# Kernel optimization log

Hardware: AMD Instinct MI355X
Metric: run time of the kernel (lower is better)

Reference implementation:

```python
import jax, jax.numpy as jnp
import numpy as np

GROUPS = 32
EPS = 1e-6

def group_norm(x, gamma, beta):
    # x: [B,C,H,W]
    B, C, H, W = x.shape
    xg = x.reshape(B, GROUPS, C // GROUPS, H, W)
    mu = xg.mean(axis=(2, 3, 4), keepdims=True)
    var = xg.var(axis=(2, 3, 4), keepdims=True)
    xn = ((xg - mu) * jax.lax.rsqrt(var + EPS)).reshape(B, C, H, W)
    return xn * gamma[None, :, None, None] + beta[None, :, None, None]

def setup_inputs() -> dict:
    key = jax.random.key(0)
    ks = jax.random.split(key, 12)
    B, C, H, W = 4, 256, 64, 64
    s = 1.0 / np.sqrt(C)
    return {
        "x": jax.random.normal(ks[0], (B, C, H, W), jnp.float32),
        "gn_gamma": jnp.ones((C,), jnp.float32),
        "gn_beta": jnp.zeros((C,), jnp.float32),
        "wq": jax.random.normal(ks[1], (C, C), jnp.float32) * s,
        "bq": jnp.zeros((C,), jnp.float32),
        "wk": jax.random.normal(ks[2], (C, C), jnp.float32) * s,
        "bk": jnp.zeros((C,), jnp.float32),
        "wv": jax.random.normal(ks[3], (C, C), jnp.float32) * s,
        "bv": jnp.zeros((C,), jnp.float32),
        "wu": jax.random.normal(ks[4], (1, C), jnp.float32) * s,
        "bu": jnp.zeros((1,), jnp.float32),
        "wp": jax.random.normal(ks[5], (C, C), jnp.float32) * s,
        "bp": jnp.zeros((C,), jnp.float32),
    }

def reference(x, gn_gamma, gn_beta, wq, bq, wk, bk, wv, bv, wu, bu, wp, bp):
    B, C, H, W = x.shape
    hw = H * W
    hn = group_norm(x, gn_gamma, gn_beta)          # norm(x); context=x so same norm
    t = hn.reshape(B, C, hw).transpose(0, 2, 1)    # [B, hw, C]
    q = t @ wq.T + bq                              # 1x1 conv == per-token linear
    k = t @ wk.T + bk
    v = t @ wv.T + bv
    u_map = jax.nn.sigmoid(t @ wu.T + bu)          # [B, hw, 1]
    scale = jnp.asarray(C, x.dtype) ** -0.5
    scores = jnp.einsum('bic,bjc->bij', q, k) * scale * u_map.transpose(0, 2, 1)
    attn = jax.nn.softmax(scores, axis=2)          # softmax over keys j
    out = jnp.einsum('bij,bjc->bic', attn, v)      # [B, hw, C]
    out = (out @ wp.T + bp).transpose(0, 2, 1).reshape(B, C, H, W)
    return (x + out, u_map)
```

## Files before the change

### kernel.cpp

```cpp
#include <hip/hip_runtime.h>
#include <cstdint>

#define B_ 4
#define C_ 256
#define HW_ 4096
#define CPG_ 8
#define M_TOT 16384
#define SCALE 0.0625f
#define LOG2E 1.44269504088896f
#define FLASH_LDS 133120

typedef __attribute__((ext_vector_type(4))) float f32x4;
typedef __attribute__((ext_vector_type(16))) float f32x16;
typedef __attribute__((ext_vector_type(8))) unsigned short u16x8;
typedef __attribute__((ext_vector_type(4))) unsigned short u16x4;
typedef __attribute__((ext_vector_type(4))) unsigned int u32x4;
typedef __attribute__((ext_vector_type(8))) __bf16 bf16x8;

static __device__ __forceinline__ unsigned short f2bf(float f) {
  unsigned int u = __builtin_bit_cast(unsigned int, f);
  u += 0x7fffu + ((u >> 16) & 1u);
  return (unsigned short)(u >> 16);
}
static __device__ __forceinline__ float bf2f(unsigned short s) {
  return __builtin_bit_cast(float, ((unsigned int)s) << 16);
}
static __device__ __forceinline__ bf16x8 ldbf8(const unsigned short* p) {
  return __builtin_bit_cast(bf16x8, *(const u16x8*)p);
}
static __device__ __forceinline__ bf16x8 cvt8(const float* p) {
  f32x4 a = *(const f32x4*)p;
  f32x4 b = *(const f32x4*)(p + 4);
  u16x8 r;
  r[0] = f2bf(a[0]); r[1] = f2bf(a[1]); r[2] = f2bf(a[2]); r[3] = f2bf(a[3]);
  r[4] = f2bf(b[0]); r[5] = f2bf(b[1]); r[6] = f2bf(b[2]); r[7] = f2bf(b[3]);
  return __builtin_bit_cast(bf16x8, r);
}
static __device__ __forceinline__ void gload16(const void* g, void* l) {
  __builtin_amdgcn_global_load_lds(
      (const __attribute__((address_space(1))) unsigned int*)g,
      (__attribute__((address_space(3))) unsigned int*)l, 16, 0, 0);
}
static __device__ __forceinline__ unsigned cvtpk(float lo, float hi) {
  unsigned r;
  asm("v_cvt_pk_bf16_f32 %0, %1, %2" : "=v"(r) : "v"(lo), "v"(hi));
  return r;
}

__global__ __launch_bounds__(256) void gn_kernel(const float* __restrict__ x,
    const float* __restrict__ gamma, const float* __restrict__ beta,
    unsigned short* __restrict__ t) {
  int bg = blockIdx.x;
  int b = bg >> 5, g = bg & 31;
  const float* xp = x + ((size_t)(b * C_ + g * CPG_)) * HW_;
  float s = 0.f, ss = 0.f;
  for (int i = threadIdx.x; i < CPG_ * HW_; i += 256) {
    float v = xp[i]; s += v; ss += v * v;
  }
#pragma unroll
  for (int m = 32; m; m >>= 1) { s += __shfl_xor(s, m); ss += __shfl_xor(ss, m); }
  __shared__ float red[8];
  if ((threadIdx.x & 63) == 0) { red[threadIdx.x >> 6] = s; red[4 + (threadIdx.x >> 6)] = ss; }
  __syncthreads();
  float S = red[0] + red[1] + red[2] + red[3];
  float SS = red[4] + red[5] + red[6] + red[7];
  float mean = S * (1.f / 32768.f);
  float var = SS * (1.f / 32768.f) - mean * mean;
  float rs = rsqrtf(var + 1e-6f);
  float gam[CPG_], bet[CPG_];
#pragma unroll
  for (int cc = 0; cc < CPG_; ++cc) {
    float gm = gamma[g * CPG_ + cc];
    gam[cc] = gm * rs;
    bet[cc] = beta[g * CPG_ + cc] - mean * gm * rs;
  }
  for (int sp = threadIdx.x; sp < HW_; sp += 256) {
    u16x8 o;
#pragma unroll
    for (int cc = 0; cc < CPG_; ++cc) {
      float v = xp[cc * HW_ + sp];
      o[cc] = f2bf(v * gam[cc] + bet[cc]);
    }
    *(u16x8*)(t + ((size_t)(b * HW_ + sp)) * C_ + g * CPG_) = o;
  }
}

__global__ __launch_bounds__(256) void u_kernel(const unsigned short* __restrict__ t,
    const float* __restrict__ wu, const float* __restrict__ bu,
    float* __restrict__ uout) {
  int w = threadIdx.x >> 6, l = threadIdx.x & 63;
  int tok = blockIdx.x * 4 + w;
  u16x4 tv = *(const u16x4*)(t + (size_t)tok * C_ + l * 4);
  f32x4 wv4 = *(const f32x4*)(wu + l * 4);
  float d = bf2f(tv[0]) * wv4[0] + bf2f(tv[1]) * wv4[1] +
            bf2f(tv[2]) * wv4[2] + bf2f(tv[3]) * wv4[3];
#pragma unroll
  for (int m = 32; m; m >>= 1) d += __shfl_xor(d, m);
  if (l == 0) uout[tok] = 1.f / (1.f + __expf(-(d + bu[0])));
}

__global__ __launch_bounds__(256, 2) void qkv_kernel(const unsigned short* __restrict__ t,
    const float* __restrict__ wq, const float* __restrict__ wk, const float* __restrict__ wv,
    const float* __restrict__ bq, const float* __restrict__ bk, const float* __restrict__ bv,
    const float* __restrict__ uu,
    unsigned short* __restrict__ q, unsigned short* __restrict__ k,
    unsigned short* __restrict__ vt) {
  int mblk = blockIdx.x, nblk = blockIdx.y;
  int n0 = nblk * 64;
  __shared__ unsigned short WL[64][264];
  __shared__ float lds[64][65];
  int tid = threadIdx.x;
  int wid = tid >> 6, l = tid & 63;
  int lr = l & 15, lg = l >> 4;
  int row = mblk * 64 + wid * 16 + lr;
  bf16x8 af[8];
  const unsigned short* ap = t + (size_t)row * C_ + lg * 8;
#pragma unroll
  for (int kc = 0; kc < 8; ++kc) af[kc] = ldbf8(ap + kc * 32);
  f32x4 u4 = *(const f32x4*)(uu + mblk * 64 + wid * 16 + lg * 4);

#pragma unroll 1
  for (int w = 0; w < 3; ++w) {
    const float* W = w == 0 ? wq : (w == 1 ? wk : wv);
    const float* bias = w == 0 ? bq : (w == 1 ? bk : bv);
    if (w) __syncthreads();
#pragma unroll
    for (int p = 0; p < 8; ++p) {
      int rw = p * 8 + (tid >> 5);
      int kc0 = (tid & 31) * 8;
      *(bf16x8*)&WL[rw][kc0] = cvt8(W + (size_t)(n0 + rw) * C_ + kc0);
    }
    __syncthreads();
    f32x4 acc[4] = {};
#pragma unroll
    for (int kc = 0; kc < 8; ++kc)
#pragma unroll
      for (int j = 0; j < 4; ++j) {
        bf16x8 bb = ldbf8(&WL[j * 16 + lr][kc * 32 + lg * 8]);
        acc[j] = __builtin_amdgcn_mfma_f32_16x16x32_bf16(af[kc], bb, acc[j], 0, 0, 0);
      }
    if (w < 2) {
      unsigned short* dst = w ? k : q;
      float su[4] = {1.f, 1.f, 1.f, 1.f};
      if (w == 1) {
        su[0] = SCALE * LOG2E * u4[0]; su[1] = SCALE * LOG2E * u4[1];
        su[2] = SCALE * LOG2E * u4[2]; su[3] = SCALE * LOG2E * u4[3];
      }
#pragma unroll
      for (int j = 0; j < 4; ++j) {
        int col = n0 + j * 16 + lr;
        float bv_ = bias[col];
#pragma unroll
        for (int r = 0; r < 4; ++r)
          dst[(size_t)(mblk * 64 + wid * 16 + lg * 4 + r) * C_ + col] =
              f2bf((acc[j][r] + bv_) * su[r]);
      }
    } else {
#pragma unroll
      for (int j = 0; j < 4; ++j) {
        float bv_ = bias[n0 + j * 16 + lr];
#pragma unroll
        for (int r = 0; r < 4; ++r)
          lds[wid * 16 + lg * 4 + r][j * 16 + lr] = acc[j][r] + bv_;
      }
      __syncthreads();
      int bb_ = (mblk * 64) >> 12;
      int s0 = (mblk * 64) & 4095;
      int ss = tid & 63, cc0 = tid >> 6;
      for (int cc = cc0; cc < 64; cc += 4)
        vt[((size_t)(bb_ * C_ + n0 + cc)) * HW_ + s0 + ss] = f2bf(lds[ss][cc]);
    }
  }
}

__global__ __launch_bounds__(512, 2) void flash_kernel(const unsigned short* __restrict__ q,
    const unsigned short* __restrict__ k, const unsigned short* __restrict__ vt,
    unsigned short* __restrict__ o) {
  extern __shared__ char smem[];
  float* cmb_m = (float*)(smem + 131072);
  float* cmb_l = (float*)(smem + 131584);
  float* facw  = (float*)(smem + 132096);
  float* scrL  = (float*)(smem + 132608);

  int blk = blockIdx.x;
  int xcd = blk & 7, slot = blk >> 3;
  int b = xcd >> 1;
  int qrow0 = (((xcd & 1) << 5) | slot) * 64;
  int tid = threadIdx.x;
  int wid = tid >> 6, l = tid & 63;
  int l5 = l & 31, hi = l >> 5;

  const unsigned short* kb = k + (size_t)b * HW_ * C_;
  const unsigned short* vb = vt + (size_t)b * C_ * HW_;

  float mrow = -1e30f, lrow = 0.f;
  f32x16 oa[8];

  if (wid >= 4) {
    int role = wid - 4;
    int sh = role & 1;
    bool isK = role < 2;
    int w_ = l >> 2;
    int w0_ = w_ & 1, w1_ = (w_ >> 1) & 1, w2_ = (w_ >> 2) & 1, w3_ = (w_ >> 3) & 1;
    int koffb = (l & 3) * 8;
#define STG(IT, BUFN)                                                           \
    {                                                                           \
      int key0n = sh * 2048 + (IT) * 32;                                        \
      if (isK) {                                                                \
        _Pragma("unroll")                                                       \
        for (int j = 0; j < 16; ++j) {                                          \
          int key = j * 2 + hi;                                                 \
          const unsigned short* g =                                             \
              kb + (size_t)(key0n + key) * C_ + ((l5 * 8) ^ (key * 8));         \
          gload16(g, smem + (BUFN) * 32768 + sh * 16384 + j * 1024);            \
        }                                                                       \
      } else {                                                                  \
        _Pragma("unroll")                                                       \
        for (int j = 0; j < 16; ++j) {                                          \
          int j0 = j & 1;                                                       \
          int ch = (j << 4) | (w3_ << 3) | ((w2_ ^ j0) << 2) |                  \
                   ((w1_ ^ w3_) << 1) | (w0_ ^ w2_ ^ j0);                       \
          int ke = koffb ^ ((ch & 3) << 3);                                     \
          const unsigned short* g = vb + (size_t)ch * HW_ + key0n + ke;         \
          gload16(g, smem + 65536 + (BUFN) * 32768 + sh * 16384 + j * 1024);    \
        }                                                                       \
      }                                                                         \
    }
    STG(0, 0);
    __syncthreads();
    for (int it = 0; it < 64; ++it) {
      if (it + 1 < 64) STG(it + 1, (it + 1) & 1);
      __syncthreads();
    }
#undef STG
  } else {
    int h = wid >> 1, qs = wid & 1;
    bf16x8 qreg[16];
    {
      const unsigned short* qp =
          q + ((size_t)b * HW_ + qrow0 + qs * 32 + l5) * C_ + hi * 8;
#pragma unroll
      for (int cc = 0; cc < 16; ++cc) qreg[cc] = ldbf8(qp + cc * 16);
    }
#pragma unroll
    for (int ct = 0; ct < 8; ++ct)
#pragma unroll
      for (int r = 0; r < 16; ++r) oa[ct][r] = 0.f;
    __syncthreads();

    int kx = l5 << 4;
    int vbase = (l5 * 64) ^ ((l5 >> 2) << 6);
    int ko0 = (hi * 16) ^ ((l & 3) << 4);
    int ko1 = (32 + hi * 16) ^ ((l & 3) << 4);

    for (int it = 0; it < 64; ++it) {
      int buf = it & 1;
      const char* KB = smem + buf * 32768 + h * 16384;
      f32x16 sa, sb;
#pragma unroll
      for (int r = 0; r < 16; ++r) { sa[r] = 0.f; sb[r] = 0.f; }
#pragma unroll
      for (int cc = 0; cc < 16; cc += 2) {
        bf16x8 kf0 = ldbf8((const unsigned short*)(KB + l5 * 512 +
                                                   ((cc * 32 + hi * 16) ^ kx)));
        bf16x8 kf1 = ldbf8((const unsigned short*)(KB + l5 * 512 +
                                                   (((cc + 1) * 32 + hi * 16) ^ kx)));
        sa = __builtin_amdgcn_mfma_f32_32x32x16_bf16(kf0, qreg[cc], sa, 0, 0, 0);
        sb = __builtin_amdgcn_mfma_f32_32x32x16_bf16(kf1, qreg[cc + 1], sb, 0, 0, 0);
      }
      f32x16 s = sa + sb;
      float mxl = s[0];
#pragma unroll
      for (int r = 1; r < 16; ++r) mxl = fmaxf(mxl, s[r]);
      float mx = fmaxf(mxl, __shfl_xor(mxl, 32));
      if (!__all(mx <= mrow + 11.f)) {
        float mnew = fmaxf(mrow, mx);
        float scr = exp2f(mrow - mnew);
        mrow = mnew;
        lrow *= scr;
        if (hi == 0) scrL[wid * 32 + l5] = scr;
        float sr[16];
#pragma unroll
        for (int r = 0; r < 16; ++r)
          sr[r] = scrL[wid * 32 + (r & 3) + 8 * (r >> 2) + 4 * hi];
#pragma unroll
        for (int ct = 0; ct < 8; ++ct)
#pragma unroll
          for (int r = 0; r < 16; ++r) oa[ct][r] *= sr[r];
      }
      unsigned wp[8];
#pragma unroll
      for (int rp = 0; rp < 8; ++rp) {
        float e0 = exp2f(s[2 * rp] - mrow);
        float e1 = exp2f(s[2 * rp + 1] - mrow);
        lrow += e0 + e1;
        wp[rp] = cvtpk(e0, e1);
      }
      unsigned sx[8];
#pragma unroll
      for (int rp = 0; rp < 8; ++rp) sx[rp] = (unsigned)__shfl_xor((int)wp[rp], 32);
      bool hib = (hi != 0);
      u32x4 pa0u = {hib ? sx[2] : wp[0], hib ? sx[3] : wp[1],
                    hib ? wp[2] : sx[0], hib ? wp[3] : sx[1]};
      u32x4 pa1u = {hib ? sx[6] : wp[4], hib ? sx[7] : wp[5],
                    hib ? wp[6] : sx[4], hib ? wp[7] : sx[5]};
      bf16x8 pa0 = __builtin_bit_cast(bf16x8, pa0u);
      bf16x8 pa1 = __builtin_bit_cast(bf16x8, pa1u);
      const char* VB = smem + 65536 + buf * 32768 + h * 16384;
#pragma unroll
      for (int ct = 0; ct < 8; ++ct) {
        bf16x8 v0 = ldbf8((const unsigned short*)(VB + ct * 2048 + vbase + ko0));
        bf16x8 v1 = ldbf8((const unsigned short*)(VB + ct * 2048 + vbase + ko1));
        oa[ct] = __builtin_amdgcn_mfma_f32_32x32x16_bf16(pa0, v0, oa[ct], 0, 0, 0);
        oa[ct] = __builtin_amdgcn_mfma_f32_32x32x16_bf16(pa1, v1, oa[ct], 0, 0, 0);
      }
      __syncthreads();
    }
  }

  float l_all = 0.f;
  if (wid < 4) {
    l_all = lrow + __shfl_xor(lrow, 32);
    if (hi == 0) { cmb_m[wid * 32 + l5] = mrow; cmb_l[wid * 32 + l5] = l_all; }
  }
  __syncthreads();
  if (wid < 4) {
    float mo = cmb_m[(wid ^ 2) * 32 + l5];
    float lo = cmb_l[(wid ^ 2) * 32 + l5];
    float M = fmaxf(mrow, mo);
    float el = exp2f(mrow - M), eo = exp2f(mo - M);
    float fac = el / (l_all * el + lo * eo);
    if (hi == 0) facw[wid * 32 + l5] = fac;
    float fr[16];
#pragma unroll
    for (int r = 0; r < 16; ++r)
      fr[r] = facw[wid * 32 + (r & 3) + 8 * (r >> 2) + 4 * hi];
    float* Ow = (float*)(smem + wid * 32768);
#pragma unroll
    for (int ct = 0; ct < 8; ++ct)
#pragma unroll
      for (int r = 0; r < 16; ++r) {
        int qr = (r & 3) + 8 * (r >> 2) + 4 * hi;
        Ow[qr * 256 + ct * 32 + l5] = oa[ct][r] * fr[r];
      }
  }
  __syncthreads();
  for (int e = tid; e < 2048; e += 512) {
    int row = e >> 5;
    int c8 = (e & 31) * 8;
    int qs_ = row >> 5, q_ = row & 31;
    const float* p0 = (const float*)(smem + qs_ * 32768) + q_ * 256 + c8;
    const float* p1 = (const float*)(smem + (2 + qs_) * 32768) + q_ * 256 + c8;
    u16x8 ov;
#pragma unroll
    for (int j = 0; j < 8; ++j) ov[j] = f2bf(p0[j] + p1[j]);
    *(u16x8*)(o + ((size_t)b * HW_ + qrow0 + row) * C_ + c8) = ov;
  }
}

__global__ __launch_bounds__(256, 2) void proj_kernel(const unsigned short* __restrict__ o,
    const float* __restrict__ wp, const float* __restrict__ bp,
    const float* __restrict__ x, float* __restrict__ y) {
  int mblk = blockIdx.x, nblk = blockIdx.y;
  int n0 = nblk * 64;
  __shared__ unsigned short WL[64][264];
  int tid = threadIdx.x;
#pragma unroll
  for (int p = 0; p < 8; ++p) {
    int row = p * 8 + (tid >> 5);
    int kc0 = (tid & 31) * 8;
    *(bf16x8*)&WL[row][kc0] = cvt8(wp + (size_t)(n0 + row) * C_ + kc0);
  }
  __syncthreads();
  int wid = tid >> 6, l = tid & 63;
  int lr = l & 15, lg = l >> 4;
  int row = mblk * 64 + wid * 16 + lr;
  f32x4 acc[4] = {};
  const unsigned short* ap = o + (size_t)row * C_ + lg * 8;
#pragma unroll
  for (int kc = 0; kc < 8; ++kc) {
    bf16x8 a = ldbf8(ap + kc * 32);
#pragma unroll
    for (int j = 0; j < 4; ++j) {
      bf16x8 bb = ldbf8(&WL[j * 16 + lr][kc * 32 + lg * 8]);
      acc[j] = __builtin_amdgcn_mfma_f32_16x16x32_bf16(a, bb, acc[j], 0, 0, 0);
    }
  }
  __shared__ float lds[64][65];
#pragma unroll
  for (int j = 0; j < 4; ++j) {
    float bv_ = bp[n0 + j * 16 + lr];
#pragma unroll
    for (int r = 0; r < 4; ++r)
      lds[wid * 16 + lg * 4 + r][j * 16 + lr] = acc[j][r] + bv_;
  }
  __syncthreads();
  int bb_ = (mblk * 64) >> 12;
  int s0 = (mblk * 64) & 4095;
  int ss = tid & 63, cc0 = tid >> 6;
  for (int cc = cc0; cc < 64; cc += 4) {
    size_t idx = ((size_t)(bb_ * C_ + n0 + cc)) * HW_ + s0 + ss;
    y[idx] = x[idx] + lds[ss][cc];
  }
}

extern "C" void kernel_launch(void* const* d_in, const int* in_sizes, int n_in,
                              void* d_out, int out_size, void* d_ws, size_t ws_size,
                              hipStream_t stream) {
  const float* x     = (const float*)d_in[0];
  const float* gamma = (const float*)d_in[1];
  const float* beta  = (const float*)d_in[2];
  const float* wq    = (const float*)d_in[3];
  const float* bq    = (const float*)d_in[4];
  const float* wk    = (const float*)d_in[5];
  const float* bk    = (const float*)d_in[6];
  const float* wv    = (const float*)d_in[7];
  const float* bv    = (const float*)d_in[8];
  const float* wu    = (const float*)d_in[9];
  const float* bu    = (const float*)d_in[10];
  const float* wp    = (const float*)d_in[11];
  const float* bp    = (const float*)d_in[12];

  float* y = (float*)d_out;
  float* uout = y + (size_t)B_ * C_ * HW_;

  unsigned short* t  = (unsigned short*)d_ws;
  unsigned short* qb = t + (size_t)M_TOT * C_;
  unsigned short* kk = qb + (size_t)M_TOT * C_;
  unsigned short* vt = kk + (size_t)M_TOT * C_;

  hipFuncSetAttribute((const void*)flash_kernel,
                      hipFuncAttributeMaxDynamicSharedMemorySize, FLASH_LDS);

  gn_kernel<<<128, 256, 0, stream>>>(x, gamma, beta, t);
  u_kernel<<<4096, 256, 0, stream>>>(t, wu, bu, uout);
  qkv_kernel<<<dim3(256, 4), 256, 0, stream>>>(t, wq, wk, wv, bq, bk, bv, uout, qb, kk, vt);
  flash_kernel<<<256, 512, FLASH_LDS, stream>>>(qb, kk, vt, t);
  proj_kernel<<<dim3(256, 4), 256, 0, stream>>>(t, wp, bp, x, y);
}
```

Measured before the change: 197.1 us.

## Split group norm into stats and apply, tune flash loop scheduling

Group norm is split into a per-group statistics kernel and a tiled apply kernel that transposes through LDS, so the token-major bf16 writes are coalesced. The flash kernel now maps blocks linearly to batch and query tile instead of using the XCD-aware mapping. It raises wave priority around MFMA sections, uses a single accumulator chain for QK^T, and reduces the row max as a tree. Exponentials are now computed before the rescale check, so they are recomputed when the max changes; the scratch scale buffer is reused for GN coefficients before u is written.

```diff
diff --git a/kernel.cpp b/kernel.cpp
--- a/kernel.cpp
+++ b/kernel.cpp
@@ -47,9 +47,9 @@
   return r;
 }
 
-__global__ __launch_bounds__(256) void gn_kernel(const float* __restrict__ x,
+__global__ __launch_bounds__(256) void gn_stats(const float* __restrict__ x,
     const float* __restrict__ gamma, const float* __restrict__ beta,
-    unsigned short* __restrict__ t) {
+    float* __restrict__ gnab) {
   int bg = blockIdx.x;
   int b = bg >> 5, g = bg & 31;
   const float* xp = x + ((size_t)(b * C_ + g * CPG_)) * HW_;
@@ -62,26 +62,45 @@
   __shared__ float red[8];
   if ((threadIdx.x & 63) == 0) { red[threadIdx.x >> 6] = s; red[4 + (threadIdx.x >> 6)] = ss; }
   __syncthreads();
-  float S = red[0] + red[1] + red[2] + red[3];
-  float SS = red[4] + red[5] + red[6] + red[7];
-  float mean = S * (1.f / 32768.f);
-  float var = SS * (1.f / 32768.f) - mean * mean;
-  float rs = rsqrtf(var + 1e-6f);
-  float gam[CPG_], bet[CPG_];
-#pragma unroll
-  for (int cc = 0; cc < CPG_; ++cc) {
-    float gm = gamma[g * CPG_ + cc];
-    gam[cc] = gm * rs;
-    bet[cc] = beta[g * CPG_ + cc] - mean * gm * rs;
-  }
-  for (int sp = threadIdx.x; sp < HW_; sp += 256) {
+  if (threadIdx.x < CPG_) {
+    float S = red[0] + red[1] + red[2] + red[3];
+    float SS = red[4] + red[5] + red[6] + red[7];
+    float mean = S * (1.f / 32768.f);
+    float var = SS * (1.f / 32768.f) - mean * mean;
+    float rs = rsqrtf(var + 1e-6f);
+    int c = g * CPG_ + threadIdx.x;
+    float gm = gamma[c];
+    gnab[b * C_ + c] = gm * rs;
+    gnab[1024 + b * C_ + c] = beta[c] - mean * gm * rs;
+  }
+}
+
+__global__ __launch_bounds__(256) void gn_apply(const float* __restrict__ x,
+    const float* __restrict__ gnab, unsigned short* __restrict__ t) {
+  __shared__ unsigned short T[64][264];
+  int blk = blockIdx.x;
+  int b = blk >> 6;
+  int sp0 = (blk & 63) * 64;
+  int tid = threadIdx.x;
+  int l = tid & 63, w = tid >> 6;
+  const float* xb = x + (size_t)b * C_ * HW_;
+  const float* ga = gnab + b * C_;
+  const float* gb = gnab + 1024 + b * C_;
+  for (int c0 = w * 64; c0 < w * 64 + 64; c0 += 8) {
     u16x8 o;
 #pragma unroll
-    for (int cc = 0; cc < CPG_; ++cc) {
-      float v = xp[cc * HW_ + sp];
-      o[cc] = f2bf(v * gam[cc] + bet[cc]);
-    }
-    *(u16x8*)(t + ((size_t)(b * HW_ + sp)) * C_ + g * CPG_) = o;
+    for (int j = 0; j < 8; ++j) {
+      int c = c0 + j;
+      float v = xb[(size_t)c * HW_ + sp0 + l];
+      o[j] = f2bf(v * ga[c] + gb[c]);
+    }
+    *(u16x8*)&T[l][c0] = o;
+  }
+  __syncthreads();
+  for (int e = tid; e < 64 * 32; e += 256) {
+    int row = e >> 5, c8 = (e & 31) * 8;
+    *(u16x8*)(t + ((size_t)(b * HW_ + sp0 + row)) * C_ + c8) =
+        *(const u16x8*)&T[row][c8];
   }
 }
 
@@ -183,9 +202,8 @@
   float* scrL  = (float*)(smem + 132608);
 
   int blk = blockIdx.x;
-  int xcd = blk & 7, slot = blk >> 3;
-  int b = xcd >> 1;
-  int qrow0 = (((xcd & 1) << 5) | slot) * 64;
+  int b = blk >> 6;
+  int qrow0 = (blk & 63) * 64;
   int tid = threadIdx.x;
   int wid = tid >> 6, l = tid & 63;
   int l5 = l & 31, hi = l >> 5;
@@ -256,23 +274,28 @@
     for (int it = 0; it < 64; ++it) {
       int buf = it & 1;
       const char* KB = smem + buf * 32768 + h * 16384;
-      f32x16 sa, sb;
-#pragma unroll
-      for (int r = 0; r < 16; ++r) { sa[r] = 0.f; sb[r] = 0.f; }
-#pragma unroll
-      for (int cc = 0; cc < 16; cc += 2) {
-        bf16x8 kf0 = ldbf8((const unsigned short*)(KB + l5 * 512 +
-                                                   ((cc * 32 + hi * 16) ^ kx)));
-        bf16x8 kf1 = ldbf8((const unsigned short*)(KB + l5 * 512 +
-                                                   (((cc + 1) * 32 + hi * 16) ^ kx)));
-        sa = __builtin_amdgcn_mfma_f32_32x32x16_bf16(kf0, qreg[cc], sa, 0, 0, 0);
-        sb = __builtin_amdgcn_mfma_f32_32x32x16_bf16(kf1, qreg[cc + 1], sb, 0, 0, 0);
-      }
-      f32x16 s = sa + sb;
-      float mxl = s[0];
-#pragma unroll
-      for (int r = 1; r < 16; ++r) mxl = fmaxf(mxl, s[r]);
+      f32x16 s;
+#pragma unroll
+      for (int r = 0; r < 16; ++r) s[r] = 0.f;
+      __builtin_amdgcn_s_setprio(1);
+#pragma unroll
+      for (int cc = 0; cc < 16; ++cc) {
+        bf16x8 kf = ldbf8((const unsigned short*)(KB + l5 * 512 +
+                                                  ((cc * 32 + hi * 16) ^ kx)));
+        s = __builtin_amdgcn_mfma_f32_32x32x16_bf16(kf, qreg[cc], s, 0, 0, 0);
+      }
+      __builtin_amdgcn_s_setprio(0);
+      float a0 = fmaxf(s[0], s[1]),   a1 = fmaxf(s[2], s[3]);
+      float a2 = fmaxf(s[4], s[5]),   a3 = fmaxf(s[6], s[7]);
+      float a4 = fmaxf(s[8], s[9]),   a5 = fmaxf(s[10], s[11]);
+      float a6 = fmaxf(s[12], s[13]), a7 = fmaxf(s[14], s[15]);
+      float b0 = fmaxf(fmaxf(a0, a1), fmaxf(a2, a3));
+      float b1 = fmaxf(fmaxf(a4, a5), fmaxf(a6, a7));
+      float mxl = fmaxf(b0, b1);
       float mx = fmaxf(mxl, __shfl_xor(mxl, 32));
+      float e[16];
+#pragma unroll
+      for (int r = 0; r < 16; ++r) e[r] = exp2f(s[r] - mrow);
       if (!__all(mx <= mrow + 11.f)) {
         float mnew = fmaxf(mrow, mx);
         float scr = exp2f(mrow - mnew);
@@ -287,14 +310,14 @@
         for (int ct = 0; ct < 8; ++ct)
 #pragma unroll
           for (int r = 0; r < 16; ++r) oa[ct][r] *= sr[r];
+#pragma unroll
+        for (int r = 0; r < 16; ++r) e[r] = exp2f(s[r] - mrow);
       }
       unsigned wp[8];
 #pragma unroll
       for (int rp = 0; rp < 8; ++rp) {
-        float e0 = exp2f(s[2 * rp] - mrow);
-        float e1 = exp2f(s[2 * rp + 1] - mrow);
-        lrow += e0 + e1;
-        wp[rp] = cvtpk(e0, e1);
+        lrow += e[2 * rp] + e[2 * rp + 1];
+        wp[rp] = cvtpk(e[2 * rp], e[2 * rp + 1]);
       }
       unsigned sx[8];
 #pragma unroll
@@ -307,6 +330,7 @@
       bf16x8 pa0 = __builtin_bit_cast(bf16x8, pa0u);
       bf16x8 pa1 = __builtin_bit_cast(bf16x8, pa1u);
       const char* VB = smem + 65536 + buf * 32768 + h * 16384;
+      __builtin_amdgcn_s_setprio(1);
 #pragma unroll
       for (int ct = 0; ct < 8; ++ct) {
         bf16x8 v0 = ldbf8((const unsigned short*)(VB + ct * 2048 + vbase + ko0));
@@ -314,10 +338,12 @@
         oa[ct] = __builtin_amdgcn_mfma_f32_32x32x16_bf16(pa0, v0, oa[ct], 0, 0, 0);
         oa[ct] = __builtin_amdgcn_mfma_f32_32x32x16_bf16(pa1, v1, oa[ct], 0, 0, 0);
       }
+      __builtin_amdgcn_s_setprio(0);
       __syncthreads();
     }
   }
 
+  int h = wid >> 1, qs = wid & 1;
   float l_all = 0.f;
   if (wid < 4) {
     l_all = lrow + __shfl_xor(lrow, 32);
@@ -432,7 +458,8 @@
   hipFuncSetAttribute((const void*)flash_kernel,
                       hipFuncAttributeMaxDynamicSharedMemorySize, FLASH_LDS);
 
-  gn_kernel<<<128, 256, 0, stream>>>(x, gamma, beta, t);
+  gn_stats<<<128, 256, 0, stream>>>(x, gamma, beta, uout);
+  gn_apply<<<256, 256, 0, stream>>>(x, uout, t);
   u_kernel<<<4096, 256, 0, stream>>>(t, wu, bu, uout);
   qkv_kernel<<<dim3(256, 4), 256, 0, stream>>>(t, wq, wk, wv, bq, bk, bv, uout, qb, kk, vt);
   flash_kernel<<<256, 512, FLASH_LDS, stream>>>(qb, kk, vt, t);
```

New measurement: 196.0 us. About the same (-0.6%).
